# Optimization experiments

Hardware: AMD Instinct MI355X
Metric: run time of the kernel (lower is better)

## Reference

```python
import jax, jax.numpy as jnp
import numpy as np

B, CIN, COUT, H, W = 8, 64, 64, 128, 128


def conv2d(x, w, b):
    # NCHW x OIHW -> NCHW, stride 1, SAME padding (kernel 3, pad 1)
    y = jax.lax.conv_general_dilated(
        x, w, window_strides=(1, 1), padding='SAME',
        dimension_numbers=('NCHW', 'OIHW', 'NCHW'))
    return y + b[None, :, None, None]


def bilinear_sample(img, py, px):
    # img: [B, C, H, W]; py, px: [B, K, H, W] float sample coords (y, x)
    # Zero padding outside the image (torchvision DeformConv2d semantics).
    Bn, C, Hn, Wn = img.shape
    y0 = jnp.floor(py)
    x0 = jnp.floor(px)
    wy = py - y0  # [B, K, H, W]
    wx = px - x0
    flat = img.reshape(Bn, C, Hn * Wn)

    def corner(yi, xi):
        valid = (yi >= 0) & (yi < Hn) & (xi >= 0) & (xi < Wn)
        yc = jnp.clip(yi, 0, Hn - 1).astype(jnp.int32)
        xc = jnp.clip(xi, 0, Wn - 1).astype(jnp.int32)
        idx = (yc * Wn + xc).reshape(Bn, -1)  # [B, K*H*W]
        g = jax.vmap(lambda f, i: f[:, i])(flat, idx)  # [B, C, K*H*W]
        g = g.reshape(Bn, C, *py.shape[1:])  # [B, C, K, H, W]
        return g * valid[:, None].astype(img.dtype)

    g00 = corner(y0, x0)
    g01 = corner(y0, x0 + 1)
    g10 = corner(y0 + 1, x0)
    g11 = corner(y0 + 1, x0 + 1)
    wy_ = wy[:, None]  # [B, 1, K, H, W]
    wx_ = wx[:, None]
    return (1 - wy_) * ((1 - wx_) * g00 + wx_ * g01) + wy_ * ((1 - wx_) * g10 + wx_ * g11)


def setup_inputs() -> dict:
    key = jax.random.key(0)
    ks = jax.random.split(key, 4)
    x = jax.random.normal(ks[0], (B, CIN, H, W), dtype=jnp.float32)
    # offset conv: in_channels -> 18 (= 2 * 3 * 3), kernel 3, pad 1
    offset_w = jax.random.normal(ks[1], (18, CIN, 3, 3), dtype=jnp.float32) * 0.01
    offset_b = jnp.zeros((18,), dtype=jnp.float32)
    deform_w = jax.random.normal(ks[2], (COUT, CIN, 3, 3), dtype=jnp.float32) * (1.0 / np.sqrt(CIN * 9))
    deform_b = jnp.zeros((COUT,), dtype=jnp.float32)
    return {'x': x, 'offset_w': offset_w, 'offset_b': offset_b,
            'deform_w': deform_w, 'deform_b': deform_b}


def reference(x, offset_w, offset_b, deform_w, deform_b):
    Bn, C, Hn, Wn = x.shape
    # 1) offset conv
    off = conv2d(x, offset_w, offset_b)  # [B, 18, H, W]
    off = off.reshape(Bn, 9, 2, Hn, Wn)  # per kernel position k: (dy, dx)
    dy = off[:, :, 0]  # [B, 9, H, W]
    dx = off[:, :, 1]
    # 2) sampling positions: p0 + p_k + offset (kernel 3x3, pad 1 -> p_k in {-1,0,1})
    k = jnp.arange(9)
    ki = (k // 3 - 1).astype(jnp.float32)[None, :, None, None]
    kj = (k % 3 - 1).astype(jnp.float32)[None, :, None, None]
    py = jnp.arange(Hn, dtype=jnp.float32)[None, None, :, None] + ki + dy
    px = jnp.arange(Wn, dtype=jnp.float32)[None, None, None, :] + kj + dx
    sampled = bilinear_sample(x, py, px)  # [B, C, 9, H, W]
    # 3) conv accumulation over (C, k)
    w = deform_w.reshape(deform_w.shape[0], C, 9)  # [O, C, 9]
    out = jnp.einsum('bckhw,ock->bohw', sampled, w) + deform_b[None, :, None, None]
    return jax.nn.relu(out)
```

## Files before the change

kernel.cpp:

```cpp
#include <hip/hip_runtime.h>
#include <hip/hip_bf16.h>

#define H_ 128
#define W_ 128
#define B_ 8
#define CIN_ 64
#define COUT_ 64

typedef __attribute__((ext_vector_type(8))) short bf16x8;
typedef __attribute__((ext_vector_type(4))) float f32x4;
typedef __attribute__((ext_vector_type(4))) unsigned int u32x4;

static __device__ __forceinline__ unsigned short f2bf(float f) {
  union { float f; unsigned int u; } a; a.f = f;
  unsigned int u = a.u;
  return (unsigned short)((u + 0x7fffu + ((u >> 16) & 1u)) >> 16);
}

static __device__ __forceinline__ unsigned int cvt_pk_bf16(float lo, float hi) {
  unsigned int r;
  asm("v_cvt_pk_bf16_f32 %0, %1, %2" : "=v"(r) : "v"(lo), "v"(hi));
  return r;
}

__global__ __launch_bounds__(256) void prep_w(const float* __restrict__ dw,
    const float* __restrict__ ow, unsigned short* __restrict__ dwt,
    unsigned short* __restrict__ owt) {
  int id = blockIdx.x * 256 + threadIdx.x;
  if (id < 36864) {
    int c = id & 63, o = (id >> 6) & 63, k = id >> 12;
    dwt[id] = f2bf(dw[(o * 64 + c) * 9 + k]);
  } else if (id < 36864 + 18432) {
    int j = id - 36864;
    int c = j & 63, om = (j >> 6) & 31, t = j >> 11;
    owt[j] = f2bf(om < 18 ? ow[(om * 64 + c) * 9 + t] : 0.f);
  }
}


__global__ __launch_bounds__(256, 4) void deform_main(const float* __restrict__ x,
    const unsigned short* __restrict__ owt, const float* __restrict__ ob,
    const unsigned short* __restrict__ dwt, const float* __restrict__ db,
    float* __restrict__ out) {
  __shared__ unsigned short ldsx[240 * 64];

  const int tid = threadIdx.x;
  const int blk = ((blockIdx.x & 7) << 8) | (blockIdx.x >> 3);
  const int b = blk >> 8;
  const int ty = ((blk >> 4) & 15) << 3;
  const int tx = (blk & 15) << 3;
  const int oy = ty - 3, ox = tx - 4;
  const int lane = tid & 63;
  const int wv = tid >> 6;
  const int pl = lane & 15;
  const int kgrp = lane >> 4;
  const int pwl = (wv << 4) | pl;
  const int pyy = ty + (pwl >> 3), pxx = tx + (pwl & 7);

  {
    int pt = tid;
    if (pt < 240) {
      int gy = oy + (pt >> 4), gx = ox + (pt & 15);
      bool ok = ((unsigned)gy < (unsigned)H_) && ((unsigned)gx < (unsigned)W_);
      int base = ((b * CIN_) * H_ + gy) * W_ + gx;
#pragma unroll
      for (int c8 = 0; c8 < 8; ++c8) {
        float v[8];
#pragma unroll
        for (int ci = 0; ci < 8; ++ci)
          v[ci] = ok ? x[base + ((c8 << 3) + ci) * (H_ * W_)] : 0.f;
        u32x4 sv;
#pragma unroll
        for (int j = 0; j < 4; ++j) sv[j] = cvt_pk_bf16(v[2 * j], v[2 * j + 1]);
        *(u32x4*)&ldsx[(pt << 6) | ((c8 ^ (pt & 7)) << 3)] = sv;
      }
    }
  }
  __syncthreads();

  float ow0, ow1, ow2, ow3, owA, owB;
  {
    f32x4 aoff0 = (f32x4){0.f, 0.f, 0.f, 0.f};
    f32x4 aoff1 = (f32x4){0.f, 0.f, 0.f, 0.f};
#pragma unroll
    for (int t = 0; t < 9; ++t) {
      const int ly = (pwl >> 3) + (t / 3) - 1 + 3;
      const int lx = (pwl & 7) + (t % 3) - 1 + 4;
      const int pt = (ly << 4) | lx;
#pragma unroll
      for (int hf = 0; hf < 2; ++hf) {
        const int c8 = (hf << 2) | kgrp;
        bf16x8 bfr = *(const bf16x8*)&ldsx[(pt << 6) | ((c8 ^ (pt & 7)) << 3)];
        bf16x8 a0 = *(const bf16x8*)&owt[(((t << 5) | pl) << 6) | (c8 << 3)];
        bf16x8 a1 = *(const bf16x8*)&owt[(((t << 5) | 16 | pl) << 6) | (c8 << 3)];
        aoff0 = __builtin_amdgcn_mfma_f32_16x16x32_bf16(a0, bfr, aoff0, 0, 0, 0);
        aoff1 = __builtin_amdgcn_mfma_f32_16x16x32_bf16(a1, bfr, aoff1, 0, 0, 0);
      }
    }
    ow0 = aoff0[0] + ob[(kgrp << 2) + 0];
    ow1 = aoff0[1] + ob[(kgrp << 2) + 1];
    ow2 = aoff0[2] + ob[(kgrp << 2) + 2];
    ow3 = aoff0[3] + ob[(kgrp << 2) + 3];
    owA = aoff1[0] + ob[16];
    owB = aoff1[1] + ob[17];
  }

  float dyk[9], dxk[9];
#pragma unroll
  for (int k = 0; k < 8; ++k) {
    int src = ((k >> 1) << 4) | pl;
    dyk[k] = __shfl((k & 1) ? ow2 : ow0, src, 64);
    dxk[k] = __shfl((k & 1) ? ow3 : ow1, src, 64);
  }
  dyk[8] = __shfl(owA, pl, 64);
  dxk[8] = __shfl(owB, pl, 64);

  f32x4 acc[4];
#pragma unroll
  for (int mt = 0; mt < 4; ++mt) acc[mt] = (f32x4){0.f, 0.f, 0.f, 0.f};

#pragma unroll
  for (int k = 0; k < 9; ++k) {
    bf16x8 af[2][4];
#pragma unroll
    for (int hf = 0; hf < 2; ++hf)
#pragma unroll
      for (int mt = 0; mt < 4; ++mt)
        af[hf][mt] = *(const bf16x8*)&dwt[(k << 12) + (((mt << 4) | pl) << 6)
                                          + (hf << 5) + (kgrp << 3)];

    const float py = (float)(pyy + (k / 3) - 1) + dyk[k];
    const float px = (float)(pxx + (k % 3) - 1) + dxk[k];
    const float fy = floorf(py), fx = floorf(px);
    const int iy = (int)fy, ix = (int)fx;
    const float wy = py - fy, wx = px - fx;
    const float wy1 = 1.f - wy, wx1 = 1.f - wx;
    const bool ry0 = (unsigned)iy < (unsigned)H_;
    const bool ry1 = (unsigned)(iy + 1) < (unsigned)H_;
    const bool rx0 = (unsigned)ix < (unsigned)W_;
    const bool rx1 = (unsigned)(ix + 1) < (unsigned)W_;
    const float w00 = (ry0 & rx0) ? wy1 * wx1 : 0.f;
    const float w01 = (ry0 & rx1) ? wy1 * wx : 0.f;
    const float w10 = (ry1 & rx0) ? wy * wx1 : 0.f;
    const float w11 = (ry1 & rx1) ? wy * wx : 0.f;

    const int ly = iy - oy, lx = ix - ox;
    const int lyc = min(max(ly, 0), 13);
    const int lxc = min(max(lx, 0), 14);
    const bool oob = (ly != lyc) | (lx != lxc);
    const int pt00 = (lyc << 4) | lxc;

    float s0[8], s1[8];
#pragma unroll
    for (int hf = 0; hf < 2; ++hf) {
      const int c8 = (hf << 2) | kgrp;
      float* s = hf ? s1 : s0;
      const unsigned short* l00 = &ldsx[(pt00 << 6) | ((c8 ^ (pt00 & 7)) << 3)];
      const unsigned short* l01 = &ldsx[((pt00 + 1) << 6) | ((c8 ^ ((pt00 + 1) & 7)) << 3)];
      const unsigned short* l10 = &ldsx[((pt00 + 16) << 6) | ((c8 ^ ((pt00 + 16) & 7)) << 3)];
      const unsigned short* l11 = &ldsx[((pt00 + 17) << 6) | ((c8 ^ ((pt00 + 17) & 7)) << 3)];
      u32x4 q00 = *(const u32x4*)l00;
      u32x4 q01 = *(const u32x4*)l01;
      u32x4 q10 = *(const u32x4*)l10;
      u32x4 q11 = *(const u32x4*)l11;
#pragma unroll
      for (int j = 0; j < 4; ++j) {
        float e = __uint_as_float(q00[j] << 16) * w00;
        e = fmaf(__uint_as_float(q01[j] << 16), w01, e);
        e = fmaf(__uint_as_float(q10[j] << 16), w10, e);
        e = fmaf(__uint_as_float(q11[j] << 16), w11, e);
        float o = __uint_as_float(q00[j] & 0xffff0000u) * w00;
        o = fmaf(__uint_as_float(q01[j] & 0xffff0000u), w01, o);
        o = fmaf(__uint_as_float(q10[j] & 0xffff0000u), w10, o);
        o = fmaf(__uint_as_float(q11[j] & 0xffff0000u), w11, o);
        s[2 * j] = e;
        s[2 * j + 1] = o;
      }
    }

    if (__builtin_expect(__ballot(oob) != 0ull, 0)) {
      if (oob) {
        int y0 = min(max(iy, 0), H_ - 1), x0 = min(max(ix, 0), W_ - 1);
        int y1 = min(max(iy + 1, 0), H_ - 1), x1 = min(max(ix + 1, 0), W_ - 1);
#pragma unroll
        for (int hf = 0; hf < 2; ++hf) {
          float* s = hf ? s1 : s0;
          const float* xp = x + (size_t)(b * CIN_ + (((hf << 2) | kgrp) << 3)) * (H_ * W_);
          for (int ci = 0; ci < 8; ++ci) {
            const float* xc = xp + ci * (H_ * W_);
            s[ci] = xc[y0 * W_ + x0] * w00 + xc[y0 * W_ + x1] * w01 +
                    xc[y1 * W_ + x0] * w10 + xc[y1 * W_ + x1] * w11;
          }
        }
      }
    }

    union { bf16x8 v; u32x4 w; } bf0, bf1;
#pragma unroll
    for (int j = 0; j < 4; ++j) {
      bf0.w[j] = cvt_pk_bf16(s0[2 * j], s0[2 * j + 1]);
      bf1.w[j] = cvt_pk_bf16(s1[2 * j], s1[2 * j + 1]);
    }
#pragma unroll
    for (int mt = 0; mt < 4; ++mt)
      acc[mt] = __builtin_amdgcn_mfma_f32_16x16x32_bf16(af[0][mt], bf0.v, acc[mt], 0, 0, 0);
#pragma unroll
    for (int mt = 0; mt < 4; ++mt)
      acc[mt] = __builtin_amdgcn_mfma_f32_16x16x32_bf16(af[1][mt], bf1.v, acc[mt], 0, 0, 0);
  }

#pragma unroll
  for (int mt = 0; mt < 4; ++mt) {
#pragma unroll
    for (int j = 0; j < 4; ++j) {
      int o = (mt << 4) | (kgrp << 2) | j;
      float v = acc[mt][j] + db[o];
      out[((b * COUT_ + o) * H_ + pyy) * W_ + pxx] = v > 0.f ? v : 0.f;
    }
  }
}

extern "C" void kernel_launch(void* const* d_in, const int* in_sizes, int n_in,
                              void* d_out, int out_size, void* d_ws, size_t ws_size,
                              hipStream_t stream) {
  const float* x  = (const float*)d_in[0];
  const float* ow = (const float*)d_in[1];
  const float* ob = (const float*)d_in[2];
  const float* dw = (const float*)d_in[3];
  const float* db = (const float*)d_in[4];
  float* out = (float*)d_out;

  unsigned short* dwt = (unsigned short*)d_ws;
  unsigned short* owt = (unsigned short*)((char*)d_ws + 73728);

  hipLaunchKernelGGL(prep_w, dim3(216), dim3(256), 0, stream, dw, ow, dwt, owt);
  hipLaunchKernelGGL(deform_main, dim3(2048), dim3(256), 0, stream,
                     x, owt, ob, dwt, db, out);
}
```

Before: 190.6 us.

## Software-pipeline LDS gathers and move out-of-tile fallback to a correction pass

Double-buffers the LDS loads in both the offset-conv MFMA loop and the deformable sampling loop, issuing the next tap's loads before consuming the current one. Sampling positions are precomputed per tap, and the rare out-of-tile path becomes a separate post-loop pass. That pass adds a correction term, the exact global-memory sample minus the wrong LDS sample, through extra MFMAs, so the main loop has no branch. Occupancy hint lowered from 4 to 3 waves per SIMD to allow more registers for the buffered data, at the cost of fewer resident waves and a slight numerical difference from the bf16 delta correction.

```diff
diff --git a/kernel.cpp b/kernel.cpp
--- a/kernel.cpp
+++ b/kernel.cpp
@@ -38,7 +38,7 @@
 }
 
 
-__global__ __launch_bounds__(256, 4) void deform_main(const float* __restrict__ x,
+__global__ __launch_bounds__(256, 3) void deform_main(const float* __restrict__ x,
     const unsigned short* __restrict__ owt, const float* __restrict__ ob,
     const unsigned short* __restrict__ dwt, const float* __restrict__ db,
     float* __restrict__ out) {
@@ -82,20 +82,32 @@
   {
     f32x4 aoff0 = (f32x4){0.f, 0.f, 0.f, 0.f};
     f32x4 aoff1 = (f32x4){0.f, 0.f, 0.f, 0.f};
+    bf16x8 sa0[2][2], sa1[2][2];
+    u32x4 sb[2][2];
+
+#define LOAD1(t, par) do { \
+    const int ly1 = (pwl >> 3) + ((t) / 3) - 1 + 3; \
+    const int lx1 = (pwl & 7) + ((t) % 3) - 1 + 4; \
+    const int ptt = (ly1 << 4) | lx1; \
+    _Pragma("unroll") for (int hf = 0; hf < 2; ++hf) { \
+      const int c8 = (hf << 2) | kgrp; \
+      sb[par][hf] = *(const u32x4*)&ldsx[(ptt << 6) | ((c8 ^ (ptt & 7)) << 3)]; \
+      sa0[par][hf] = *(const bf16x8*)&owt[((((t) << 5) | pl) << 6) | (c8 << 3)]; \
+      sa1[par][hf] = *(const bf16x8*)&owt[((((t) << 5) | 16 | pl) << 6) | (c8 << 3)]; \
+    } } while (0)
+
+#define CONS1(t, par) do { \
+    _Pragma("unroll") for (int hf = 0; hf < 2; ++hf) { \
+      union { u32x4 w; bf16x8 v; } bu; bu.w = sb[par][hf]; \
+      aoff0 = __builtin_amdgcn_mfma_f32_16x16x32_bf16(sa0[par][hf], bu.v, aoff0, 0, 0, 0); \
+      aoff1 = __builtin_amdgcn_mfma_f32_16x16x32_bf16(sa1[par][hf], bu.v, aoff1, 0, 0, 0); \
+    } } while (0)
+
+    LOAD1(0, 0);
 #pragma unroll
     for (int t = 0; t < 9; ++t) {
-      const int ly = (pwl >> 3) + (t / 3) - 1 + 3;
-      const int lx = (pwl & 7) + (t % 3) - 1 + 4;
-      const int pt = (ly << 4) | lx;
-#pragma unroll
-      for (int hf = 0; hf < 2; ++hf) {
-        const int c8 = (hf << 2) | kgrp;
-        bf16x8 bfr = *(const bf16x8*)&ldsx[(pt << 6) | ((c8 ^ (pt & 7)) << 3)];
-        bf16x8 a0 = *(const bf16x8*)&owt[(((t << 5) | pl) << 6) | (c8 << 3)];
-        bf16x8 a1 = *(const bf16x8*)&owt[(((t << 5) | 16 | pl) << 6) | (c8 << 3)];
-        aoff0 = __builtin_amdgcn_mfma_f32_16x16x32_bf16(a0, bfr, aoff0, 0, 0, 0);
-        aoff1 = __builtin_amdgcn_mfma_f32_16x16x32_bf16(a1, bfr, aoff1, 0, 0, 0);
-      }
+      if (t < 8) LOAD1(t + 1, (t + 1) & 1);
+      CONS1(t, t & 1);
     }
     ow0 = aoff0[0] + ob[(kgrp << 2) + 0];
     ow1 = aoff0[1] + ob[(kgrp << 2) + 1];
@@ -115,98 +127,147 @@
   dyk[8] = __shfl(owA, pl, 64);
   dxk[8] = __shfl(owB, pl, 64);
 
+  int ptk[9];
+  unsigned oobbits = 0;
+#pragma unroll
+  for (int k = 0; k < 9; ++k) {
+    float py = (float)(pyy + (k / 3) - 1) + dyk[k];
+    float px = (float)(pxx + (k % 3) - 1) + dxk[k];
+    int iy = (int)floorf(py), ix = (int)floorf(px);
+    int ly = iy - oy, lx = ix - ox;
+    int lyc = min(max(ly, 0), 13), lxc = min(max(lx, 0), 14);
+    oobbits |= ((ly != lyc) | (lx != lxc)) ? (1u << k) : 0u;
+    ptk[k] = (lyc << 4) | lxc;
+  }
+
   f32x4 acc[4];
 #pragma unroll
   for (int mt = 0; mt < 4; ++mt) acc[mt] = (f32x4){0.f, 0.f, 0.f, 0.f};
 
+  u32x4 q[2][8];
+
+#define LOADQ(kk, par) do { \
+    const int pt00 = ptk[kk]; \
+    _Pragma("unroll") for (int hf = 0; hf < 2; ++hf) { \
+      const int c8 = (hf << 2) | kgrp; \
+      _Pragma("unroll") for (int cr = 0; cr < 4; ++cr) { \
+        const int ptc = pt00 + ((cr >> 1) << 4) + (cr & 1); \
+        q[par][hf * 4 + cr] = *(const u32x4*)&ldsx[(ptc << 6) | ((c8 ^ (ptc & 7)) << 3)]; \
+      } } } while (0)
+
+#define CONSQ(kk, par) do { \
+    bf16x8 af0[4], af1[4]; \
+    _Pragma("unroll") for (int mt = 0; mt < 4; ++mt) { \
+      af0[mt] = *(const bf16x8*)&dwt[((kk) << 12) + (((mt << 4) | pl) << 6) + (kgrp << 3)]; \
+      af1[mt] = *(const bf16x8*)&dwt[((kk) << 12) + (((mt << 4) | pl) << 6) + 32 + (kgrp << 3)]; \
+    } \
+    const float py = (float)(pyy + ((kk) / 3) - 1) + dyk[kk]; \
+    const float px = (float)(pxx + ((kk) % 3) - 1) + dxk[kk]; \
+    const float fy = floorf(py), fx = floorf(px); \
+    const int iy = (int)fy, ix = (int)fx; \
+    const float wy = py - fy, wx = px - fx; \
+    const float wy1 = 1.f - wy, wx1 = 1.f - wx; \
+    const bool ry0 = (unsigned)iy < (unsigned)H_; \
+    const bool ry1 = (unsigned)(iy + 1) < (unsigned)H_; \
+    const bool rx0 = (unsigned)ix < (unsigned)W_; \
+    const bool rx1 = (unsigned)(ix + 1) < (unsigned)W_; \
+    const float w00 = (ry0 & rx0) ? wy1 * wx1 : 0.f; \
+    const float w01 = (ry0 & rx1) ? wy1 * wx : 0.f; \
+    const float w10 = (ry1 & rx0) ? wy * wx1 : 0.f; \
+    const float w11 = (ry1 & rx1) ? wy * wx : 0.f; \
+    union { bf16x8 v; u32x4 w; } bfr0, bfr1; \
+    _Pragma("unroll") for (int hf = 0; hf < 2; ++hf) { \
+      _Pragma("unroll") for (int j = 0; j < 4; ++j) { \
+        const unsigned a00 = q[par][hf * 4 + 0][j], a01 = q[par][hf * 4 + 1][j]; \
+        const unsigned a10 = q[par][hf * 4 + 2][j], a11 = q[par][hf * 4 + 3][j]; \
+        float e = __uint_as_float(a00 << 16) * w00; \
+        e = fmaf(__uint_as_float(a01 << 16), w01, e); \
+        e = fmaf(__uint_as_float(a10 << 16), w10, e); \
+        e = fmaf(__uint_as_float(a11 << 16), w11, e); \
+        float o = __uint_as_float(a00 & 0xffff0000u) * w00; \
+        o = fmaf(__uint_as_float(a01 & 0xffff0000u), w01, o); \
+        o = fmaf(__uint_as_float(a10 & 0xffff0000u), w10, o); \
+        o = fmaf(__uint_as_float(a11 & 0xffff0000u), w11, o); \
+        if (hf == 0) bfr0.w[j] = cvt_pk_bf16(e, o); else bfr1.w[j] = cvt_pk_bf16(e, o); \
+      } } \
+    _Pragma("unroll") for (int mt = 0; mt < 4; ++mt) \
+      acc[mt] = __builtin_amdgcn_mfma_f32_16x16x32_bf16(af0[mt], bfr0.v, acc[mt], 0, 0, 0); \
+    _Pragma("unroll") for (int mt = 0; mt < 4; ++mt) \
+      acc[mt] = __builtin_amdgcn_mfma_f32_16x16x32_bf16(af1[mt], bfr1.v, acc[mt], 0, 0, 0); \
+  } while (0)
+
+  LOADQ(0, 0);
 #pragma unroll
   for (int k = 0; k < 9; ++k) {
-    bf16x8 af[2][4];
-#pragma unroll
-    for (int hf = 0; hf < 2; ++hf)
-#pragma unroll
-      for (int mt = 0; mt < 4; ++mt)
-        af[hf][mt] = *(const bf16x8*)&dwt[(k << 12) + (((mt << 4) | pl) << 6)
-                                          + (hf << 5) + (kgrp << 3)];
-
-    const float py = (float)(pyy + (k / 3) - 1) + dyk[k];
-    const float px = (float)(pxx + (k % 3) - 1) + dxk[k];
-    const float fy = floorf(py), fx = floorf(px);
-    const int iy = (int)fy, ix = (int)fx;
-    const float wy = py - fy, wx = px - fx;
-    const float wy1 = 1.f - wy, wx1 = 1.f - wx;
-    const bool ry0 = (unsigned)iy < (unsigned)H_;
-    const bool ry1 = (unsigned)(iy + 1) < (unsigned)H_;
-    const bool rx0 = (unsigned)ix < (unsigned)W_;
-    const bool rx1 = (unsigned)(ix + 1) < (unsigned)W_;
-    const float w00 = (ry0 & rx0) ? wy1 * wx1 : 0.f;
-    const float w01 = (ry0 & rx1) ? wy1 * wx : 0.f;
-    const float w10 = (ry1 & rx0) ? wy * wx1 : 0.f;
-    const float w11 = (ry1 & rx1) ? wy * wx : 0.f;
-
-    const int ly = iy - oy, lx = ix - ox;
-    const int lyc = min(max(ly, 0), 13);
-    const int lxc = min(max(lx, 0), 14);
-    const bool oob = (ly != lyc) | (lx != lxc);
-    const int pt00 = (lyc << 4) | lxc;
-
-    float s0[8], s1[8];
-#pragma unroll
-    for (int hf = 0; hf < 2; ++hf) {
-      const int c8 = (hf << 2) | kgrp;
-      float* s = hf ? s1 : s0;
-      const unsigned short* l00 = &ldsx[(pt00 << 6) | ((c8 ^ (pt00 & 7)) << 3)];
-      const unsigned short* l01 = &ldsx[((pt00 + 1) << 6) | ((c8 ^ ((pt00 + 1) & 7)) << 3)];
-      const unsigned short* l10 = &ldsx[((pt00 + 16) << 6) | ((c8 ^ ((pt00 + 16) & 7)) << 3)];
-      const unsigned short* l11 = &ldsx[((pt00 + 17) << 6) | ((c8 ^ ((pt00 + 17) & 7)) << 3)];
-      u32x4 q00 = *(const u32x4*)l00;
-      u32x4 q01 = *(const u32x4*)l01;
-      u32x4 q10 = *(const u32x4*)l10;
-      u32x4 q11 = *(const u32x4*)l11;
-#pragma unroll
-      for (int j = 0; j < 4; ++j) {
-        float e = __uint_as_float(q00[j] << 16) * w00;
-        e = fmaf(__uint_as_float(q01[j] << 16), w01, e);
-        e = fmaf(__uint_as_float(q10[j] << 16), w10, e);
-        e = fmaf(__uint_as_float(q11[j] << 16), w11, e);
-        float o = __uint_as_float(q00[j] & 0xffff0000u) * w00;
-        o = fmaf(__uint_as_float(q01[j] & 0xffff0000u), w01, o);
-        o = fmaf(__uint_as_float(q10[j] & 0xffff0000u), w10, o);
-        o = fmaf(__uint_as_float(q11[j] & 0xffff0000u), w11, o);
-        s[2 * j] = e;
-        s[2 * j + 1] = o;
-      }
-    }
-
-    if (__builtin_expect(__ballot(oob) != 0ull, 0)) {
-      if (oob) {
-        int y0 = min(max(iy, 0), H_ - 1), x0 = min(max(ix, 0), W_ - 1);
-        int y1 = min(max(iy + 1, 0), H_ - 1), x1 = min(max(ix + 1, 0), W_ - 1);
-#pragma unroll
+    if (k < 8) LOADQ(k + 1, (k + 1) & 1);
+    CONSQ(k, k & 1);
+  }
+
+  if (__builtin_expect(__ballot(oobbits != 0u) != 0ull, 0)) {
+#pragma unroll 1
+    for (int k = 0; k < 9; ++k) {
+      if (__ballot((oobbits >> k) & 1u) != 0ull) {
+        const bool mine = ((oobbits >> k) & 1u) != 0u;
+        const float py = (float)(pyy + (k / 3) - 1) + dyk[k];
+        const float px = (float)(pxx + (k % 3) - 1) + dxk[k];
+        const float fy = floorf(py), fx = floorf(px);
+        const int iy = (int)fy, ix = (int)fx;
+        const float wy = py - fy, wx = px - fx;
+        const float wy1 = 1.f - wy, wx1 = 1.f - wx;
+        const bool ry0 = (unsigned)iy < (unsigned)H_;
+        const bool ry1 = (unsigned)(iy + 1) < (unsigned)H_;
+        const bool rx0 = (unsigned)ix < (unsigned)W_;
+        const bool rx1 = (unsigned)(ix + 1) < (unsigned)W_;
+        const float w00 = (ry0 & rx0) ? wy1 * wx1 : 0.f;
+        const float w01 = (ry0 & rx1) ? wy1 * wx : 0.f;
+        const float w10 = (ry1 & rx0) ? wy * wx1 : 0.f;
+        const float w11 = (ry1 & rx1) ? wy * wx : 0.f;
+        const int y0 = min(max(iy, 0), H_ - 1), x0c = min(max(ix, 0), W_ - 1);
+        const int y1 = min(max(iy + 1, 0), H_ - 1), x1c = min(max(ix + 1, 0), W_ - 1);
+        const int pt00 = ptk[k];
+#pragma unroll 1
         for (int hf = 0; hf < 2; ++hf) {
-          float* s = hf ? s1 : s0;
-          const float* xp = x + (size_t)(b * CIN_ + (((hf << 2) | kgrp) << 3)) * (H_ * W_);
-          for (int ci = 0; ci < 8; ++ci) {
-            const float* xc = xp + ci * (H_ * W_);
-            s[ci] = xc[y0 * W_ + x0] * w00 + xc[y0 * W_ + x1] * w01 +
-                    xc[y1 * W_ + x0] * w10 + xc[y1 * W_ + x1] * w11;
+          const int c8 = (hf << 2) | kgrp;
+          u32x4 qq[4];
+#pragma unroll
+          for (int cr = 0; cr < 4; ++cr) {
+            const int ptc = pt00 + ((cr >> 1) << 4) + (cr & 1);
+            qq[cr] = *(const u32x4*)&ldsx[(ptc << 6) | ((c8 ^ (ptc & 7)) << 3)];
+          }
+          const float* xb = x + (size_t)(b * CIN_ + (c8 << 3)) * (H_ * W_);
+          union { bf16x8 v; u32x4 w; } dfr;
+#pragma unroll
+          for (int j = 0; j < 4; ++j) {
+            float d[2];
+#pragma unroll
+            for (int e2 = 0; e2 < 2; ++e2) {
+              const int ci = 2 * j + e2;
+              const unsigned sh = e2 ? 0u : 16u;
+              const unsigned msk = e2 ? 0xffff0000u : 0u;
+              float wrong;
+              {
+                float s = __uint_as_float(e2 ? (qq[0][j] & msk) : (qq[0][j] << sh)) * w00;
+                s = fmaf(__uint_as_float(e2 ? (qq[1][j] & msk) : (qq[1][j] << sh)), w01, s);
+                s = fmaf(__uint_as_float(e2 ? (qq[2][j] & msk) : (qq[2][j] << sh)), w10, s);
+                s = fmaf(__uint_as_float(e2 ? (qq[3][j] & msk) : (qq[3][j] << sh)), w11, s);
+                wrong = s;
+              }
+              const float* xc = xb + (size_t)ci * (H_ * W_);
+              float right = xc[y0 * W_ + x0c] * w00 + xc[y0 * W_ + x1c] * w01 +
+                            xc[y1 * W_ + x0c] * w10 + xc[y1 * W_ + x1c] * w11;
+              d[e2] = mine ? (right - wrong) : 0.f;
+            }
+            dfr.w[j] = cvt_pk_bf16(d[0], d[1]);
+          }
+#pragma unroll
+          for (int mt = 0; mt < 4; ++mt) {
+            bf16x8 a = *(const bf16x8*)&dwt[(k << 12) + (((mt << 4) | pl) << 6)
+                                            + (hf << 5) + (kgrp << 3)];
+            acc[mt] = __builtin_amdgcn_mfma_f32_16x16x32_bf16(a, dfr.v, acc[mt], 0, 0, 0);
           }
         }
       }
     }
-
-    union { bf16x8 v; u32x4 w; } bf0, bf1;
-#pragma unroll
-    for (int j = 0; j < 4; ++j) {
-      bf0.w[j] = cvt_pk_bf16(s0[2 * j], s0[2 * j + 1]);
-      bf1.w[j] = cvt_pk_bf16(s1[2 * j], s1[2 * j + 1]);
-    }
-#pragma unroll
-    for (int mt = 0; mt < 4; ++mt)
-      acc[mt] = __builtin_amdgcn_mfma_f32_16x16x32_bf16(af[0][mt], bf0.v, acc[mt], 0, 0, 0);
-#pragma unroll
-    for (int mt = 0; mt < 4; ++mt)
-      acc[mt] = __builtin_amdgcn_mfma_f32_16x16x32_bf16(af[1][mt], bf1.v, acc[mt], 0, 0, 0);
   }
 
 #pragma unroll
```

After: 200.2 us. 1.05x slower.

## Split channel halves across two wave groups with LDS reduction of accumulators

Applied to the files above, without the earlier changes.

Doubles the block to 512 threads: the two groups of four waves each handle half of the input channels for the same 16-pixel tile, so each wave does half the bilinear sampling and MFMA work. The partial accumulators are then summed through LDS before the bias, ReLU and store. The out-of-tile fallback now runs after the main loop as a correction term: the global-memory sample minus the clamped LDS sample goes through an extra MFMA. The LDS tile fill is also spread over all 512 threads. The aim is more waves per tile for latency hiding and less register pressure per wave, at the cost of an extra reduction, two barriers, and the fallback correction being rounded to bf16.

```diff
diff --git a/kernel.cpp b/kernel.cpp
--- a/kernel.cpp
+++ b/kernel.cpp
@@ -38,11 +38,11 @@
 }
 
 
-__global__ __launch_bounds__(256, 4) void deform_main(const float* __restrict__ x,
+__global__ __launch_bounds__(512, 6) void deform_main(const float* __restrict__ x,
     const unsigned short* __restrict__ owt, const float* __restrict__ ob,
     const unsigned short* __restrict__ dwt, const float* __restrict__ db,
     float* __restrict__ out) {
-  __shared__ unsigned short ldsx[240 * 64];
+  __shared__ __attribute__((aligned(16))) unsigned short ldsx[240 * 64];
 
   const int tid = threadIdx.x;
   const int blk = ((blockIdx.x & 7) << 8) | (blockIdx.x >> 3);
@@ -52,28 +52,30 @@
   const int oy = ty - 3, ox = tx - 4;
   const int lane = tid & 63;
   const int wv = tid >> 6;
+  const int pg = wv & 3;
+  const int wvh = wv >> 2;
   const int pl = lane & 15;
   const int kgrp = lane >> 4;
-  const int pwl = (wv << 4) | pl;
+  const int pwl = (pg << 4) | pl;
   const int pyy = ty + (pwl >> 3), pxx = tx + (pwl & 7);
-
-  {
-    int pt = tid;
+  const int mc8 = (wvh << 2) | kgrp;
+
+#pragma unroll
+  for (int i = 0; i < 4; ++i) {
+    int u = (i << 9) + tid;
+    int pt = u & 255, sc8 = u >> 8;
     if (pt < 240) {
       int gy = oy + (pt >> 4), gx = ox + (pt & 15);
       bool ok = ((unsigned)gy < (unsigned)H_) && ((unsigned)gx < (unsigned)W_);
-      int base = ((b * CIN_) * H_ + gy) * W_ + gx;
-#pragma unroll
-      for (int c8 = 0; c8 < 8; ++c8) {
-        float v[8];
-#pragma unroll
-        for (int ci = 0; ci < 8; ++ci)
-          v[ci] = ok ? x[base + ((c8 << 3) + ci) * (H_ * W_)] : 0.f;
-        u32x4 sv;
-#pragma unroll
-        for (int j = 0; j < 4; ++j) sv[j] = cvt_pk_bf16(v[2 * j], v[2 * j + 1]);
-        *(u32x4*)&ldsx[(pt << 6) | ((c8 ^ (pt & 7)) << 3)] = sv;
-      }
+      int base = ((b * CIN_ + (sc8 << 3)) * H_ + gy) * W_ + gx;
+      float v[8];
+#pragma unroll
+      for (int ci = 0; ci < 8; ++ci)
+        v[ci] = ok ? x[base + ci * (H_ * W_)] : 0.f;
+      u32x4 sv;
+#pragma unroll
+      for (int j = 0; j < 4; ++j) sv[j] = cvt_pk_bf16(v[2 * j], v[2 * j + 1]);
+      *(u32x4*)&ldsx[(pt << 6) | ((sc8 ^ (pt & 7)) << 3)] = sv;
     }
   }
   __syncthreads();
@@ -84,17 +86,18 @@
     f32x4 aoff1 = (f32x4){0.f, 0.f, 0.f, 0.f};
 #pragma unroll
     for (int t = 0; t < 9; ++t) {
-      const int ly = (pwl >> 3) + (t / 3) - 1 + 3;
-      const int lx = (pwl & 7) + (t % 3) - 1 + 4;
-      const int pt = (ly << 4) | lx;
+      const int ly1 = (pwl >> 3) + (t / 3) - 1 + 3;
+      const int lx1 = (pwl & 7) + (t % 3) - 1 + 4;
+      const int ptt = (ly1 << 4) | lx1;
 #pragma unroll
       for (int hf = 0; hf < 2; ++hf) {
         const int c8 = (hf << 2) | kgrp;
-        bf16x8 bfr = *(const bf16x8*)&ldsx[(pt << 6) | ((c8 ^ (pt & 7)) << 3)];
+        union { u32x4 w; bf16x8 v; } bu;
+        bu.w = *(const u32x4*)&ldsx[(ptt << 6) | ((c8 ^ (ptt & 7)) << 3)];
         bf16x8 a0 = *(const bf16x8*)&owt[(((t << 5) | pl) << 6) | (c8 << 3)];
         bf16x8 a1 = *(const bf16x8*)&owt[(((t << 5) | 16 | pl) << 6) | (c8 << 3)];
-        aoff0 = __builtin_amdgcn_mfma_f32_16x16x32_bf16(a0, bfr, aoff0, 0, 0, 0);
-        aoff1 = __builtin_amdgcn_mfma_f32_16x16x32_bf16(a1, bfr, aoff1, 0, 0, 0);
+        aoff0 = __builtin_amdgcn_mfma_f32_16x16x32_bf16(a0, bu.v, aoff0, 0, 0, 0);
+        aoff1 = __builtin_amdgcn_mfma_f32_16x16x32_bf16(a1, bu.v, aoff1, 0, 0, 0);
       }
     }
     ow0 = aoff0[0] + ob[(kgrp << 2) + 0];
@@ -118,17 +121,10 @@
   f32x4 acc[4];
 #pragma unroll
   for (int mt = 0; mt < 4; ++mt) acc[mt] = (f32x4){0.f, 0.f, 0.f, 0.f};
+  unsigned oobbits = 0;
 
 #pragma unroll
   for (int k = 0; k < 9; ++k) {
-    bf16x8 af[2][4];
-#pragma unroll
-    for (int hf = 0; hf < 2; ++hf)
-#pragma unroll
-      for (int mt = 0; mt < 4; ++mt)
-        af[hf][mt] = *(const bf16x8*)&dwt[(k << 12) + (((mt << 4) | pl) << 6)
-                                          + (hf << 5) + (kgrp << 3)];
-
     const float py = (float)(pyy + (k / 3) - 1) + dyk[k];
     const float px = (float)(pxx + (k % 3) - 1) + dxk[k];
     const float fy = floorf(py), fx = floorf(px);
@@ -147,75 +143,116 @@
     const int ly = iy - oy, lx = ix - ox;
     const int lyc = min(max(ly, 0), 13);
     const int lxc = min(max(lx, 0), 14);
-    const bool oob = (ly != lyc) | (lx != lxc);
+    oobbits |= ((ly != lyc) | (lx != lxc)) ? (1u << k) : 0u;
     const int pt00 = (lyc << 4) | lxc;
-
-    float s0[8], s1[8];
-#pragma unroll
-    for (int hf = 0; hf < 2; ++hf) {
-      const int c8 = (hf << 2) | kgrp;
-      float* s = hf ? s1 : s0;
-      const unsigned short* l00 = &ldsx[(pt00 << 6) | ((c8 ^ (pt00 & 7)) << 3)];
-      const unsigned short* l01 = &ldsx[((pt00 + 1) << 6) | ((c8 ^ ((pt00 + 1) & 7)) << 3)];
-      const unsigned short* l10 = &ldsx[((pt00 + 16) << 6) | ((c8 ^ ((pt00 + 16) & 7)) << 3)];
-      const unsigned short* l11 = &ldsx[((pt00 + 17) << 6) | ((c8 ^ ((pt00 + 17) & 7)) << 3)];
-      u32x4 q00 = *(const u32x4*)l00;
-      u32x4 q01 = *(const u32x4*)l01;
-      u32x4 q10 = *(const u32x4*)l10;
-      u32x4 q11 = *(const u32x4*)l11;
-#pragma unroll
-      for (int j = 0; j < 4; ++j) {
-        float e = __uint_as_float(q00[j] << 16) * w00;
-        e = fmaf(__uint_as_float(q01[j] << 16), w01, e);
-        e = fmaf(__uint_as_float(q10[j] << 16), w10, e);
-        e = fmaf(__uint_as_float(q11[j] << 16), w11, e);
-        float o = __uint_as_float(q00[j] & 0xffff0000u) * w00;
-        o = fmaf(__uint_as_float(q01[j] & 0xffff0000u), w01, o);
-        o = fmaf(__uint_as_float(q10[j] & 0xffff0000u), w10, o);
-        o = fmaf(__uint_as_float(q11[j] & 0xffff0000u), w11, o);
-        s[2 * j] = e;
-        s[2 * j + 1] = o;
-      }
-    }
-
-    if (__builtin_expect(__ballot(oob) != 0ull, 0)) {
-      if (oob) {
-        int y0 = min(max(iy, 0), H_ - 1), x0 = min(max(ix, 0), W_ - 1);
-        int y1 = min(max(iy + 1, 0), H_ - 1), x1 = min(max(ix + 1, 0), W_ - 1);
-#pragma unroll
-        for (int hf = 0; hf < 2; ++hf) {
-          float* s = hf ? s1 : s0;
-          const float* xp = x + (size_t)(b * CIN_ + (((hf << 2) | kgrp) << 3)) * (H_ * W_);
-          for (int ci = 0; ci < 8; ++ci) {
-            const float* xc = xp + ci * (H_ * W_);
-            s[ci] = xc[y0 * W_ + x0] * w00 + xc[y0 * W_ + x1] * w01 +
-                    xc[y1 * W_ + x0] * w10 + xc[y1 * W_ + x1] * w11;
+    const int pt01 = pt00 + 1, pt10 = pt00 + 16, pt11 = pt00 + 17;
+
+    u32x4 q00 = *(const u32x4*)&ldsx[(pt00 << 6) | ((mc8 ^ (pt00 & 7)) << 3)];
+    u32x4 q01 = *(const u32x4*)&ldsx[(pt01 << 6) | ((mc8 ^ (pt01 & 7)) << 3)];
+    u32x4 q10 = *(const u32x4*)&ldsx[(pt10 << 6) | ((mc8 ^ (pt10 & 7)) << 3)];
+    u32x4 q11 = *(const u32x4*)&ldsx[(pt11 << 6) | ((mc8 ^ (pt11 & 7)) << 3)];
+
+    union { bf16x8 v; u32x4 w; } bfr;
+#pragma unroll
+    for (int j = 0; j < 4; ++j) {
+      float e = __uint_as_float(q00[j] << 16) * w00;
+      e = fmaf(__uint_as_float(q01[j] << 16), w01, e);
+      e = fmaf(__uint_as_float(q10[j] << 16), w10, e);
+      e = fmaf(__uint_as_float(q11[j] << 16), w11, e);
+      float o = __uint_as_float(q00[j] & 0xffff0000u) * w00;
+      o = fmaf(__uint_as_float(q01[j] & 0xffff0000u), w01, o);
+      o = fmaf(__uint_as_float(q10[j] & 0xffff0000u), w10, o);
+      o = fmaf(__uint_as_float(q11[j] & 0xffff0000u), w11, o);
+      bfr.w[j] = cvt_pk_bf16(e, o);
+    }
+#pragma unroll
+    for (int mt = 0; mt < 4; ++mt) {
+      bf16x8 af = *(const bf16x8*)&dwt[(k << 12) + (((mt << 4) | pl) << 6)
+                                       + (wvh << 5) + (kgrp << 3)];
+      acc[mt] = __builtin_amdgcn_mfma_f32_16x16x32_bf16(af, bfr.v, acc[mt], 0, 0, 0);
+    }
+  }
+
+  if (__builtin_expect(__ballot(oobbits != 0u) != 0ull, 0)) {
+#pragma unroll 1
+    for (int k = 0; k < 9; ++k) {
+      if (__ballot((oobbits >> k) & 1u) != 0ull) {
+        const bool mine = ((oobbits >> k) & 1u) != 0u;
+        const float py = (float)(pyy + (k / 3) - 1) + dyk[k];
+        const float px = (float)(pxx + (k % 3) - 1) + dxk[k];
+        const float fy = floorf(py), fx = floorf(px);
+        const int iy = (int)fy, ix = (int)fx;
+        const float wy = py - fy, wx = px - fx;
+        const float wy1 = 1.f - wy, wx1 = 1.f - wx;
+        const bool ry0 = (unsigned)iy < (unsigned)H_;
+        const bool ry1 = (unsigned)(iy + 1) < (unsigned)H_;
+        const bool rx0 = (unsigned)ix < (unsigned)W_;
+        const bool rx1 = (unsigned)(ix + 1) < (unsigned)W_;
+        const float w00 = (ry0 & rx0) ? wy1 * wx1 : 0.f;
+        const float w01 = (ry0 & rx1) ? wy1 * wx : 0.f;
+        const float w10 = (ry1 & rx0) ? wy * wx1 : 0.f;
+        const float w11 = (ry1 & rx1) ? wy * wx : 0.f;
+        const int ly = iy - oy, lx = ix - ox;
+        const int lyc = min(max(ly, 0), 13);
+        const int lxc = min(max(lx, 0), 14);
+        const int pt00 = (lyc << 4) | lxc;
+        const int y0 = min(max(iy, 0), H_ - 1), x0c = min(max(ix, 0), W_ - 1);
+        const int y1 = min(max(iy + 1, 0), H_ - 1), x1c = min(max(ix + 1, 0), W_ - 1);
+        u32x4 qq[4];
+#pragma unroll
+        for (int cr = 0; cr < 4; ++cr) {
+          const int ptc = pt00 + ((cr >> 1) << 4) + (cr & 1);
+          qq[cr] = *(const u32x4*)&ldsx[(ptc << 6) | ((mc8 ^ (ptc & 7)) << 3)];
+        }
+        const float* xb = x + (size_t)(b * CIN_ + (mc8 << 3)) * (H_ * W_);
+        union { bf16x8 v; u32x4 w; } dfr;
+#pragma unroll
+        for (int j = 0; j < 4; ++j) {
+          float d[2];
+#pragma unroll
+          for (int e2 = 0; e2 < 2; ++e2) {
+            float s = __uint_as_float(e2 ? (qq[0][j] & 0xffff0000u) : (qq[0][j] << 16)) * w00;
+            s = fmaf(__uint_as_float(e2 ? (qq[1][j] & 0xffff0000u) : (qq[1][j] << 16)), w01, s);
+            s = fmaf(__uint_as_float(e2 ? (qq[2][j] & 0xffff0000u) : (qq[2][j] << 16)), w10, s);
+            s = fmaf(__uint_as_float(e2 ? (qq[3][j] & 0xffff0000u) : (qq[3][j] << 16)), w11, s);
+            const float* xc = xb + (size_t)(2 * j + e2) * (H_ * W_);
+            float right = xc[y0 * W_ + x0c] * w00 + xc[y0 * W_ + x1c] * w01 +
+                          xc[y1 * W_ + x0c] * w10 + xc[y1 * W_ + x1c] * w11;
+            d[e2] = mine ? (right - s) : 0.f;
           }
+          dfr.w[j] = cvt_pk_bf16(d[0], d[1]);
+        }
+#pragma unroll
+        for (int mt = 0; mt < 4; ++mt) {
+          bf16x8 a = *(const bf16x8*)&dwt[(k << 12) + (((mt << 4) | pl) << 6)
+                                          + (wvh << 5) + (kgrp << 3)];
+          acc[mt] = __builtin_amdgcn_mfma_f32_16x16x32_bf16(a, dfr.v, acc[mt], 0, 0, 0);
         }
       }
     }
-
-    union { bf16x8 v; u32x4 w; } bf0, bf1;
-#pragma unroll
-    for (int j = 0; j < 4; ++j) {
-      bf0.w[j] = cvt_pk_bf16(s0[2 * j], s0[2 * j + 1]);
-      bf1.w[j] = cvt_pk_bf16(s1[2 * j], s1[2 * j + 1]);
-    }
+  }
+
+  __syncthreads();
+  float* lred = (float*)ldsx;
+  const int xsw = (lane >> 1) & 3;
+  if (wv >= 4) {
+    const int base = (((wv - 4) << 6) | lane) << 4;
 #pragma unroll
     for (int mt = 0; mt < 4; ++mt)
-      acc[mt] = __builtin_amdgcn_mfma_f32_16x16x32_bf16(af[0][mt], bf0.v, acc[mt], 0, 0, 0);
-#pragma unroll
-    for (int mt = 0; mt < 4; ++mt)
-      acc[mt] = __builtin_amdgcn_mfma_f32_16x16x32_bf16(af[1][mt], bf1.v, acc[mt], 0, 0, 0);
-  }
-
-#pragma unroll
-  for (int mt = 0; mt < 4; ++mt) {
-#pragma unroll
-    for (int j = 0; j < 4; ++j) {
-      int o = (mt << 4) | (kgrp << 2) | j;
-      float v = acc[mt][j] + db[o];
-      out[((b * COUT_ + o) * H_ + pyy) * W_ + pxx] = v > 0.f ? v : 0.f;
+      *(f32x4*)&lred[base + ((mt ^ xsw) << 2)] = acc[mt];
+  }
+  __syncthreads();
+  if (wv < 4) {
+    const int base = ((wv << 6) | lane) << 4;
+#pragma unroll
+    for (int mt = 0; mt < 4; ++mt) {
+      f32x4 p = *(const f32x4*)&lred[base + ((mt ^ xsw) << 2)];
+#pragma unroll
+      for (int j = 0; j < 4; ++j) {
+        int o = (mt << 4) | (kgrp << 2) | j;
+        float v = acc[mt][j] + p[j] + db[o];
+        out[((b * COUT_ + o) * H_ + pyy) * W_ + pxx] = v > 0.f ? v : 0.f;
+      }
     }
   }
 }
@@ -234,6 +271,6 @@
   unsigned short* owt = (unsigned short*)((char*)d_ws + 73728);
 
   hipLaunchKernelGGL(prep_w, dim3(216), dim3(256), 0, stream, dw, ow, dwt, owt);
-  hipLaunchKernelGGL(deform_main, dim3(2048), dim3(256), 0, stream,
+  hipLaunchKernelGGL(deform_main, dim3(2048), dim3(512), 0, stream,
                      x, owt, ob, dwt, db, out);
 }
```

New measurement: 261.2 us. +37.0%, slower.
